# Performance work log

Measured on AMD Instinct MI355X. Metric: run time of the kernel, lower is better.

## Reference

```python
import jax, jax.numpy as jnp
import numpy as np

DN = ('NCDHW', 'DHWIO', 'NCDHW')


def _w(key, cin, cout):
    # kernel_size=3 in 3D, Minkowski-style fan-in scaling, no bias
    scale = 1.0 / np.sqrt(cin * 27)
    return jax.random.normal(key, (3, 3, 3, cin, cout), dtype=jnp.float32) * scale


def setup_inputs() -> dict:
    key = jax.random.key(0)
    ks = jax.random.split(key, 7)
    x = jax.random.normal(ks[0], (1, 1024, 4, 4, 4), dtype=jnp.float32)
    chans = [(1024, 512), (512, 256), (256, 128), (128, 64), (64, 32), (32, 1)]
    ws = {f'w{i+1}': _w(ks[i + 1], ci, co) for i, (ci, co) in enumerate(chans)}
    return {'x': x, **ws}


def _ct(x, w, stride):
    # conv-transpose, kernel 3, SAME padding: stride 2 doubles resolution,
    # stride 1 preserves it (dense analog of Minkowski generative transpose conv)
    return jax.lax.conv_transpose(x, w, strides=(stride, stride, stride),
                                  padding='SAME', dimension_numbers=DN)


def reference(x, w1, w2, w3, w4, w5, w6):
    h = jax.nn.relu(_ct(x, w1, 2))   # 1024 -> 512, 4^3 -> 8^3
    h = jax.nn.relu(_ct(h, w2, 1))   # 512 -> 256
    h = jax.nn.relu(_ct(h, w3, 2))   # 256 -> 128, 8^3 -> 16^3
    h = jax.nn.relu(_ct(h, w4, 1))   # 128 -> 64
    h = jax.nn.relu(_ct(h, w5, 2))   # 64 -> 32, 16^3 -> 32^3
    return _ct(h, w6, 1)             # 32 -> 1, no final ReLU
```

## Files before the change

### kernel.cpp

```cpp
#include <hip/hip_runtime.h>

typedef _Float16 half8 __attribute__((ext_vector_type(8)));
typedef _Float16 half4v __attribute__((ext_vector_type(4)));
typedef float floatx4 __attribute__((ext_vector_type(4)));


__global__ __launch_bounds__(256) void pad_x_k(const float* __restrict__ X,
                                               _Float16* __restrict__ P) {
  int idx = blockIdx.x * 256 + threadIdx.x;
  if (idx >= 125 * 1024) return;
  int c = idx & 1023;
  int r = idx >> 10;
  int px = r % 5, py = (r / 5) % 5, pz = r / 25;
  float v = 0.f;
  if (px >= 1 && py >= 1 && pz >= 1)
    v = X[c * 64 + (pz - 1) * 16 + (py - 1) * 4 + (px - 1)];
  P[idx] = (_Float16)v;
}

template <int POS, int COUT, int S2IN, int NSPL, int PS>
__device__ __forceinline__ void red_body(int vb, const float* __restrict__ Pp,
                                         _Float16* __restrict__ P) {
  constexpr int C4 = COUT / 4;
  constexpr size_t U3 =
      S2IN ? (size_t)(POS / 2) * (POS / 2) * (POS / 2) : (size_t)POS * POS * POS;
  int idx = vb * 256 + threadIdx.x;
  if (idx >= PS * PS * PS * C4) return;
  const int co = (idx % C4) * 4;
  const int r = idx / C4;
  const int px = r % PS, py = (r / PS) % PS, pz = r / (PS * PS);
  const int ix = px - 1, iy = py - 1, iz = pz - 1;
  float4 s = make_float4(0.f, 0.f, 0.f, 0.f);
  if ((unsigned)ix < (unsigned)POS && (unsigned)iy < (unsigned)POS &&
      (unsigned)iz < (unsigned)POS) {
    int j0, j1;
    size_t upos;
    if (S2IN) {
      const int pf[8] = {0, 8, 12, 16, 18, 22, 24, 26};
      const int tc[8] = {8, 4, 4, 2, 4, 2, 2, 1};
      const int cls = ((iz & 1) << 2) | ((iy & 1) << 1) | (ix & 1);
      j0 = pf[cls] * NSPL;
      j1 = j0 + tc[cls] * NSPL;
      constexpr int U = POS / 2;
      upos = ((size_t)(iz >> 1) * U + (iy >> 1)) * U + (ix >> 1);
    } else {
      j0 = 0;
      j1 = NSPL;
      upos = ((size_t)iz * POS + iy) * POS + ix;
    }
    const float* base = Pp + upos * COUT + co;
    for (int j = j0; j < j1; j++) {
      float4 v = *(const float4*)(base + (size_t)j * U3 * COUT);
      s.x += v.x; s.y += v.y; s.z += v.z; s.w += v.w;
    }
  }
  half4v h;
  h[0] = (_Float16)fmaxf(s.x, 0.f);
  h[1] = (_Float16)fmaxf(s.y, 0.f);
  h[2] = (_Float16)fmaxf(s.z, 0.f);
  h[3] = (_Float16)fmaxf(s.w, 0.f);
  *(half4v*)(P + (size_t)idx * 4) = h;
}

template <int POS, int COUT, int S2IN, int NSPL, int PS>
__global__ __launch_bounds__(256) void red_k(const float* __restrict__ Pp,
                                             _Float16* __restrict__ P) {
  red_body<POS, COUT, S2IN, NSPL, PS>(blockIdx.x, Pp, P);
}

__global__ __launch_bounds__(256) void red4z_k(const float* __restrict__ Q4,
                                               _Float16* __restrict__ P5,
                                               _Float16* __restrict__ P6) {
  if (blockIdx.x < 308) {
    red_body<16, 64, 0, 12, 17>(blockIdx.x, Q4, P5);
  } else {
    int i = (blockIdx.x - 308) * 256 + threadIdx.x;
    if (i < 157216) ((half8*)P6)[i] = half8{};
  }
}

template <int CICHUNK, int CIN, int COUT, int NTILE, int TZ, int SOUTU,
          int PS, int SMODE, int TAPG, int STORE_MODE>
__global__ __launch_bounds__(256) void conv_mfma_k(
    const _Float16* __restrict__ P, const float* __restrict__ W,
    void* __restrict__ Optr) {
  constexpr int M = TZ * 16;
  constexpr bool S2 = (SMODE != 0);
  constexpr int MTZ = SOUTU / TZ;
  constexpr int MTXY = SOUTU / 4;
  constexpr int MT3 = MTZ * MTXY * MTXY;
  constexpr int KB = 32;
  constexpr int KP = 40;
  constexpr int KBI = CICHUNK / KB;
  constexpr int NCI = CIN / CICHUNK;
  constexpr int S = S2 ? 2 * SOUTU : SOUTU;
  constexpr int WM = (M == 128) ? 4 : 2;
  constexpr int NSUB = (WM == 4) ? (NTILE / 16) : (NTILE / 32);
  constexpr int BJ = KB * NTILE / 256;
  constexpr size_t U3 = (size_t)SOUTU * SOUTU * SOUTU;

  __shared__ __align__(16) _Float16 As[M][KP];
  __shared__ __align__(16) _Float16 Bs[NTILE][KP];

  int bx = blockIdx.x;
  int cls = 0, tap0 = 0, cig = blockIdx.z, jspl = 0;
  int p_toz = 0, p_toy = 0, p_tox = 0, p_wtap = 0;
  if (SMODE == 0) {
    const int tg = cig / NCI;
    cig -= tg * NCI;
    tap0 = tg * TAPG;
    jspl = blockIdx.z;
  } else if (SMODE == 1) {
    const int p = bx / MT3;
    bx -= p * MT3;
    jspl = p * NCI + cig;
    cls = (p >= 8) + (p >= 12) + (p >= 16) + (p >= 18) + (p >= 22) +
          (p >= 24) + (p >= 26);
    const int pf = cls == 0 ? 0 : cls == 1 ? 8 : cls == 2 ? 12
                 : cls == 3 ? 16 : cls == 4 ? 18 : cls == 5 ? 22
                 : cls == 6 ? 24 : 26;
    const int tl = p - pf;
    const int lz = (cls >> 2) & 1, ly = (cls >> 1) & 1, lx = cls & 1;
    const int shx = lx ? 0 : 1, shy = ly ? 0 : 1;
    const int iz = tl >> (shx + shy);
    const int rem = tl & ((1 << (shx + shy)) - 1);
    const int iy = rem >> shx;
    const int ix = rem & ((1 << shx) - 1);
    p_toz = lz ? 1 : iz;
    p_toy = ly ? 1 : iy;
    p_tox = lx ? 1 : ix;
    const int wz = lz ? 1 : 2 * iz, wy = ly ? 1 : 2 * iy,
              wx = lx ? 1 : 2 * ix;
    p_wtap = (wz * 3 + wy) * 3 + wx;
  } else {
    cls = bx / MT3;
    bx -= cls * MT3;
  }
  const int clz = (cls >> 2) & 1, cly = (cls >> 1) & 1, clx = cls & 1;

  const int u0z = (bx / (MTXY * MTXY)) * TZ;
  const int u0y = ((bx / MTXY) % MTXY) * 4;
  const int u0x = (bx % MTXY) * 4;
  const int n_base = blockIdx.y * NTILE;

  const int t = threadIdx.x;
  const int lane = t & 63;
  const int wave = t >> 6;

  const int skq = t & 3;
  const int sp = t >> 2;
  const int spx = sp & 3, spy = (sp >> 2) & 3, spz = sp >> 4;
  const int nB = t & (NTILE - 1);
  const int k0B = (t / NTILE) * BJ;
  const int m0w = (WM == 4) ? wave * 32 : (wave >> 1) * 32;
  const int n0w = (WM == 4) ? 0 : (wave & 1) * 32;
  const int fr = lane & 15;
  const int fq = lane >> 4;

  const int cz = S2 ? (clz ? 1 : 2) : 3;
  const int cy = S2 ? (cly ? 1 : 2) : 3;
  const int cx = S2 ? (clx ? 1 : 2) : 3;
  const int shx2 = clx ? 0 : 1, shy2 = cly ? 0 : 1;

  int NIT;
  if (SMODE == 0) NIT = TAPG * KBI;
  else if (SMODE == 1) NIT = KBI;
  else NIT = cz * cy * cx * KBI;

  floatx4 acc[2][NSUB];
#pragma unroll
  for (int i = 0; i < 2; i++)
#pragma unroll
    for (int s = 0; s < NSUB; s++) acc[i][s] = {0.f, 0.f, 0.f, 0.f};

  half8 rA0 = {}, rA1 = {}, nA0 = {}, nA1 = {};
  float rB[BJ] = {}, nBv[BJ] = {};

  auto load_it = [&](int it, half8& A0, half8& A1, float* BW) {
    int tap, kb;
    if (SMODE == 1) { tap = 0; kb = it; }
    else if (KBI == 1) { tap = it; kb = 0; }
    else { tap = it / KBI; kb = it - tap * KBI; }
    int toz, toy, tox, wtap;
    if (SMODE == 1) {
      toz = p_toz; toy = p_toy; tox = p_tox; wtap = p_wtap;
    } else if (SMODE == 0) {
      const int tt = tap0 + tap;
      const int iz = tt / 9;
      const int rem = tt - iz * 9;
      const int iy = rem / 3;
      const int ix = rem - iy * 3;
      toz = iz; toy = iy; tox = ix;
      wtap = tt;
    } else {
      const int iz = tap >> (shx2 + shy2);
      const int rem = tap & ((1 << (shx2 + shy2)) - 1);
      const int iy = rem >> shx2;
      const int ix = rem & ((1 << shx2) - 1);
      toz = clz ? 1 : iz; toy = cly ? 1 : iy; tox = clx ? 1 : ix;
      const int wz = clz ? 1 : 2 * iz, wy = cly ? 1 : 2 * iy,
                wx = clx ? 1 : 2 * ix;
      wtap = (wz * 3 + wy) * 3 + wx;
    }
    const int kof0 = cig * CICHUNK + kb * KB;
    const size_t pb =
        ((size_t)(((u0z + toz + spz) * PS + (u0y + toy + spy)) * PS +
                  (u0x + tox + spx))) * CIN + kof0 + skq * 8;
    A0 = *(const half8*)(P + pb);
    if (M == 128)
      A1 = *(const half8*)(P + pb + (size_t)4 * PS * PS * CIN);
    const float* wb =
        W + ((size_t)wtap * CIN + kof0 + k0B) * COUT + n_base + nB;
#pragma unroll
    for (int j = 0; j < BJ; j++) BW[j] = wb[(size_t)j * COUT];
  };

  load_it(0, rA0, rA1, rB);

  for (int it = 0; it < NIT; ++it) {
    *(half8*)&As[sp][skq * 8] = rA0;
    if (M == 128) *(half8*)&As[sp + 64][skq * 8] = rA1;
    if (BJ == 8) {
      half8 hb;
#pragma unroll
      for (int j = 0; j < 8; j++) hb[j] = (_Float16)rB[j];
      *(half8*)&Bs[nB][k0B] = hb;
    } else {
      half4v hb;
#pragma unroll
      for (int j = 0; j < 4; j++) hb[j] = (_Float16)rB[j];
      *(half4v*)&Bs[nB][k0B] = hb;
    }
    __syncthreads();
    if (it + 1 < NIT) load_it(it + 1, nA0, nA1, nBv);
    half8 a0 = *(const half8*)&As[m0w + fr][fq * 8];
    half8 a1 = *(const half8*)&As[m0w + 16 + fr][fq * 8];
#pragma unroll
    for (int s = 0; s < NSUB; s++) {
      half8 b = *(const half8*)&Bs[n0w + s * 16 + fr][fq * 8];
      acc[0][s] = __builtin_amdgcn_mfma_f32_16x16x32_f16(a0, b, acc[0][s], 0, 0, 0);
      acc[1][s] = __builtin_amdgcn_mfma_f32_16x16x32_f16(a1, b, acc[1][s], 0, 0, 0);
    }
    __syncthreads();
    rA0 = nA0;
    rA1 = nA1;
#pragma unroll
    for (int j = 0; j < BJ; j++) rB[j] = nBv[j];
  }

#pragma unroll
  for (int i = 0; i < 2; i++) {
#pragma unroll
    for (int r = 0; r < 4; r++) {
      const int m = m0w + i * 16 + fq * 4 + r;
      const int mz = m >> 4, my = (m >> 2) & 3, mx = m & 3;
      if (STORE_MODE == 2) {
        const int oz = 2 * (u0z + mz) + clz;
        const int oy = 2 * (u0y + my) + cly;
        const int ox = 2 * (u0x + mx) + clx;
        _Float16* o = (_Float16*)Optr +
            ((size_t)(((oz + 1) * (S + 2) + (oy + 1)) * (S + 2) + (ox + 1))) *
                COUT + n_base + n0w;
#pragma unroll
        for (int s = 0; s < NSUB; s++)
          o[s * 16 + fr] = (_Float16)fmaxf(acc[i][s][r], 0.f);
      } else {
        const size_t pos =
            ((size_t)((u0z + mz) * SOUTU + (u0y + my))) * SOUTU + (u0x + mx);
        float* o = (float*)Optr + ((size_t)jspl * U3 + pos) * COUT + n_base +
                   n0w;
#pragma unroll
        for (int s = 0; s < NSUB; s++) o[s * 16 + fr] = acc[i][s][r];
      }
    }
  }
}

__global__ __launch_bounds__(128) void conv6_k(const _Float16* __restrict__ P,
                                               const float* __restrict__ W6,
                                               float* __restrict__ O) {
  __shared__ __align__(16) float w[864];
  for (int i = threadIdx.x; i < 864; i += 128) w[i] = W6[i];
  __syncthreads();
  int idx = blockIdx.x * 128 + threadIdx.x;
  int x = idx & 31, y = (idx >> 5) & 31, z = idx >> 10;
  float a = 0.f;
  for (int dz = 0; dz < 3; dz++)
    for (int dy = 0; dy < 3; dy++)
      for (int dx = 0; dx < 3; dx++) {
        const _Float16* p =
            P + (size_t)(((z + dz) * 34 + (y + dy)) * 34 + (x + dx)) * 32;
        const float* ww = &w[((dz * 3 + dy) * 3 + dx) * 32];
#pragma unroll
        for (int c = 0; c < 32; c += 8) {
          half8 pv = *(const half8*)&p[c];
#pragma unroll
          for (int u = 0; u < 8; u++) a += (float)pv[u] * ww[c + u];
        }
      }
  O[idx] = a;
}

extern "C" void kernel_launch(void* const* d_in, const int* in_sizes, int n_in,
                              void* d_out, int out_size, void* d_ws,
                              size_t ws_size, hipStream_t stream) {
  const float* x  = (const float*)d_in[0];
  const float* w1 = (const float*)d_in[1];
  const float* w2 = (const float*)d_in[2];
  const float* w3 = (const float*)d_in[3];
  const float* w4 = (const float*)d_in[4];
  const float* w5 = (const float*)d_in[5];
  const float* w6 = (const float*)d_in[6];
  float* out = (float*)d_out;

  float* Q1 = (float*)d_ws;
  float* Q2 = Q1 + 3538944;
  float* Q3 = Q2 + 3145728;
  float* Q4 = Q3 + 3538944;
  _Float16* P1 = (_Float16*)(Q4 + 3145728);
  _Float16* P2 = P1 + 128000;
  _Float16* P3 = P2 + 512000;
  _Float16* P4 = P3 + 186624;
  _Float16* P5 = P4 + 746496;
  _Float16* P6 = P5 + 314432;

  pad_x_k<<<500, 256, 0, stream>>>(x, P1);
  conv_mfma_k<256, 1024, 512, 64, 4, 4, 5, 1, 0, 3>
      <<<dim3(27, 8, 4), 256, 0, stream>>>(P1, w1, Q1);
  red_k<8, 512, 1, 4, 10><<<500, 256, 0, stream>>>(Q1, P2);
  conv_mfma_k<64, 512, 256, 64, 8, 8, 10, 0, 9, 3>
      <<<dim3(4, 4, 24), 256, 0, stream>>>(P2, w2, Q2);
  red_k<8, 256, 0, 24, 9><<<183, 256, 0, stream>>>(Q2, P3);
  conv_mfma_k<128, 256, 128, 64, 8, 8, 9, 1, 0, 3>
      <<<dim3(108, 2, 2), 256, 0, stream>>>(P3, w3, Q3);
  red_k<16, 128, 1, 2, 18><<<729, 256, 0, stream>>>(Q3, P4);
  conv_mfma_k<32, 128, 64, 64, 8, 16, 18, 0, 9, 3>
      <<<dim3(32, 1, 12), 256, 0, stream>>>(P4, w4, Q4);
  red4z_k<<<923, 256, 0, stream>>>(Q4, P5, P6);
  conv_mfma_k<64, 64, 32, 32, 8, 16, 17, 2, 0, 2>
      <<<dim3(256, 1, 1), 256, 0, stream>>>(P5, w5, P6);
  conv6_k<<<256, 128, 0, stream>>>(P6, w6, out);

  (void)in_sizes; (void)n_in; (void)out_size; (void)ws_size;
}
```

Measured before the change: 207.8 us.

## Fuse input padding into first conv and halve M-tile for later convs

Removes the separate pad/convert kernel by having the first transpose-conv gather fp32 input directly from NCDHW with bounds checks and convert it to half on the fly. The later conv launches switch from TZ=8 to TZ=4 (M tile 64), doubling block counts. NSUB and the per-wave N offset are generalized so the M=64 tile uses two waves along N. This saves a launch and a buffer round trip, and gives more parallelism in the smaller layers. The cost is strided, uncoalesced input gathers in layer 1 and less weight reuse per block in the later layers.

```diff
diff --git a/kernel.cpp b/kernel.cpp
--- a/kernel.cpp
+++ b/kernel.cpp
@@ -4,19 +4,6 @@
 typedef _Float16 half4v __attribute__((ext_vector_type(4)));
 typedef float floatx4 __attribute__((ext_vector_type(4)));
 
-
-__global__ __launch_bounds__(256) void pad_x_k(const float* __restrict__ X,
-                                               _Float16* __restrict__ P) {
-  int idx = blockIdx.x * 256 + threadIdx.x;
-  if (idx >= 125 * 1024) return;
-  int c = idx & 1023;
-  int r = idx >> 10;
-  int px = r % 5, py = (r / 5) % 5, pz = r / 25;
-  float v = 0.f;
-  if (px >= 1 && py >= 1 && pz >= 1)
-    v = X[c * 64 + (pz - 1) * 16 + (py - 1) * 4 + (px - 1)];
-  P[idx] = (_Float16)v;
-}
 
 template <int POS, int COUT, int S2IN, int NSPL, int PS>
 __device__ __forceinline__ void red_body(int vb, const float* __restrict__ Pp,
@@ -80,10 +67,10 @@
 }
 
 template <int CICHUNK, int CIN, int COUT, int NTILE, int TZ, int SOUTU,
-          int PS, int SMODE, int TAPG, int STORE_MODE>
+          int PS, int SMODE, int TAPG, int STORE_MODE, int GX>
 __global__ __launch_bounds__(256) void conv_mfma_k(
     const _Float16* __restrict__ P, const float* __restrict__ W,
-    void* __restrict__ Optr) {
+    void* __restrict__ Optr, const float* __restrict__ Xg) {
   constexpr int M = TZ * 16;
   constexpr bool S2 = (SMODE != 0);
   constexpr int MTZ = SOUTU / TZ;
@@ -95,7 +82,8 @@
   constexpr int NCI = CIN / CICHUNK;
   constexpr int S = S2 ? 2 * SOUTU : SOUTU;
   constexpr int WM = (M == 128) ? 4 : 2;
-  constexpr int NSUB = (WM == 4) ? (NTILE / 16) : (NTILE / 32);
+  constexpr int NH = (WM == 4) ? NTILE : (NTILE / 2);
+  constexpr int NSUB = NH / 16;
   constexpr int BJ = KB * NTILE / 256;
   constexpr size_t U3 = (size_t)SOUTU * SOUTU * SOUTU;
 
@@ -153,7 +141,7 @@
   const int nB = t & (NTILE - 1);
   const int k0B = (t / NTILE) * BJ;
   const int m0w = (WM == 4) ? wave * 32 : (wave >> 1) * 32;
-  const int n0w = (WM == 4) ? 0 : (wave & 1) * 32;
+  const int n0w = (WM == 4) ? 0 : (wave & 1) * NH;
   const int fr = lane & 15;
   const int fq = lane >> 4;
 
@@ -203,12 +191,30 @@
       wtap = (wz * 3 + wy) * 3 + wx;
     }
     const int kof0 = cig * CICHUNK + kb * KB;
-    const size_t pb =
-        ((size_t)(((u0z + toz + spz) * PS + (u0y + toy + spy)) * PS +
-                  (u0x + tox + spx))) * CIN + kof0 + skq * 8;
-    A0 = *(const half8*)(P + pb);
-    if (M == 128)
-      A1 = *(const half8*)(P + pb + (size_t)4 * PS * PS * CIN);
+    if (GX) {
+      const int gz = u0z + toz + spz - 1;
+      const int gy = u0y + toy + spy - 1;
+      const int gxx = u0x + tox + spx - 1;
+      const int c0 = kof0 + skq * 8;
+      if ((unsigned)gxx < (unsigned)SOUTU && (unsigned)gy < (unsigned)SOUTU &&
+          (unsigned)gz < (unsigned)SOUTU) {
+        const float* xb = Xg + (size_t)c0 * (SOUTU * SOUTU * SOUTU) +
+                          (gz * SOUTU + gy) * SOUTU + gxx;
+#pragma unroll
+        for (int u = 0; u < 8; u++)
+          A0[u] = (_Float16)xb[(size_t)u * (SOUTU * SOUTU * SOUTU)];
+      } else {
+#pragma unroll
+        for (int u = 0; u < 8; u++) A0[u] = (_Float16)0.f;
+      }
+    } else {
+      const size_t pb =
+          ((size_t)(((u0z + toz + spz) * PS + (u0y + toy + spy)) * PS +
+                    (u0x + tox + spx))) * CIN + kof0 + skq * 8;
+      A0 = *(const half8*)(P + pb);
+      if (M == 128)
+        A1 = *(const half8*)(P + pb + (size_t)4 * PS * PS * CIN);
+    }
     const float* wb =
         W + ((size_t)wtap * CIN + kof0 + k0B) * COUT + n_base + nB;
 #pragma unroll
@@ -324,21 +330,20 @@
   _Float16* P5 = P4 + 746496;
   _Float16* P6 = P5 + 314432;
 
-  pad_x_k<<<500, 256, 0, stream>>>(x, P1);
-  conv_mfma_k<256, 1024, 512, 64, 4, 4, 5, 1, 0, 3>
-      <<<dim3(27, 8, 4), 256, 0, stream>>>(P1, w1, Q1);
+  conv_mfma_k<256, 1024, 512, 64, 4, 4, 5, 1, 0, 3, 1>
+      <<<dim3(27, 8, 4), 256, 0, stream>>>(nullptr, w1, Q1, x);
   red_k<8, 512, 1, 4, 10><<<500, 256, 0, stream>>>(Q1, P2);
-  conv_mfma_k<64, 512, 256, 64, 8, 8, 10, 0, 9, 3>
-      <<<dim3(4, 4, 24), 256, 0, stream>>>(P2, w2, Q2);
+  conv_mfma_k<64, 512, 256, 64, 4, 8, 10, 0, 9, 3, 0>
+      <<<dim3(8, 4, 24), 256, 0, stream>>>(P2, w2, Q2, nullptr);
   red_k<8, 256, 0, 24, 9><<<183, 256, 0, stream>>>(Q2, P3);
-  conv_mfma_k<128, 256, 128, 64, 8, 8, 9, 1, 0, 3>
-      <<<dim3(108, 2, 2), 256, 0, stream>>>(P3, w3, Q3);
+  conv_mfma_k<128, 256, 128, 64, 4, 8, 9, 1, 0, 3, 0>
+      <<<dim3(216, 2, 2), 256, 0, stream>>>(P3, w3, Q3, nullptr);
   red_k<16, 128, 1, 2, 18><<<729, 256, 0, stream>>>(Q3, P4);
-  conv_mfma_k<32, 128, 64, 64, 8, 16, 18, 0, 9, 3>
-      <<<dim3(32, 1, 12), 256, 0, stream>>>(P4, w4, Q4);
+  conv_mfma_k<32, 128, 64, 64, 4, 16, 18, 0, 9, 3, 0>
+      <<<dim3(64, 1, 12), 256, 0, stream>>>(P4, w4, Q4, nullptr);
   red4z_k<<<923, 256, 0, stream>>>(Q4, P5, P6);
-  conv_mfma_k<64, 64, 32, 32, 8, 16, 17, 2, 0, 2>
-      <<<dim3(256, 1, 1), 256, 0, stream>>>(P5, w5, P6);
+  conv_mfma_k<64, 64, 32, 32, 4, 16, 17, 2, 0, 2, 0>
+      <<<dim3(512, 1, 1), 256, 0, stream>>>(P5, w5, P6, nullptr);
   conv6_k<<<256, 128, 0, stream>>>(P6, w6, out);
 
   (void)in_sizes; (void)n_in; (void)out_size; (void)ws_size;
```

Result: no change. 206.8 us (-0.5%).
